# Performance work log

Hardware: AMD Instinct MI355X
Metric: run time of the kernel (lower is better)

## Reference

```python
import jax, jax.numpy as jnp
import numpy as np

IOU_THRESHOLD = 0.5  # default iou_threshold of nms/class_spec_nms


def _nms_keep_mask(boxes, scores, iou_threshold):
    """Faithful port of the hand-rolled greedy NMS.

    The torch version builds a variable-length index list; here we return the
    equivalent fixed-shape boolean keep mask over the N boxes (jit-friendly).
    """
    n = scores.shape[0]
    x1, y1, x2, y2 = boxes[:, 0], boxes[:, 1], boxes[:, 2], boxes[:, 3]
    areas = (x2 - x1) * (y2 - y1)                       # [N]
    # pairwise intersection via broadcasted min/max (same math as the matmul-
    # with-ones trick in the source, without materializing the ones matrices)
    xi = jnp.minimum(x2[:, None], x2[None, :]) - jnp.maximum(x1[:, None], x1[None, :])
    yi = jnp.minimum(y2[:, None], y2[None, :]) - jnp.maximum(y1[:, None], y1[None, :])
    inter = jnp.maximum(xi, 0.0) * jnp.maximum(yi, 0.0)  # [N,N]
    iou = inter / (areas[:, None] + areas[None, :] - inter)

    first_max = scores.max()
    first_min = scores.min()
    curr_idx0 = jnp.argmax(scores)

    # carry: (candidate mask, working scores copy, keep mask, curr max, curr idx)
    init = (scores < first_max, scores, jnp.zeros((n,), dtype=bool), first_max, curr_idx0)

    def cond(state):
        mask, _, _, cmax, _ = state
        return jnp.any(mask) & (cmax >= first_min)

    def body(state):
        mask, sc, keep, cmax, cidx = state
        mask = mask & (iou[cidx] <= iou_threshold)   # suppress overlaps with current max
        mask = mask.at[cidx].set(False)
        keep = keep.at[cidx].set(True)               # keep current max
        sc = jnp.where(mask, sc, first_min - 1.0)    # kill suppressed scores
        cidx = jnp.argmax(sc)
        return mask, sc, keep, sc[cidx], cidx

    _, _, keep, _, _ = jax.lax.while_loop(cond, body, init)
    return keep


def setup_inputs() -> dict:
    key = jax.random.key(0)
    k1, k2, k3, k4, k5, k6 = jax.random.split(key, 6)
    N = 4096    # pre-NMS candidate boxes
    L = 16384   # p3 locations for a 1024x1024 image at stride 8 (128*128)
    xy = jax.random.uniform(k1, (N, 2), dtype=jnp.float32) * 900.0
    wh = jax.random.uniform(k2, (N, 2), dtype=jnp.float32) * 100.0 + 1.0
    boxes = jnp.concatenate([xy, xy + wh], axis=1)          # valid x1<x2, y1<y2
    scores = jax.random.uniform(k3, (N,), dtype=jnp.float32)
    class_ids = jax.random.randint(k4, (N,), 0, 80, dtype=jnp.int32)
    locations = jax.random.uniform(k5, (L, 2), dtype=jnp.float32) * 1024.0
    deltas = jax.random.uniform(k6, (L, 4), dtype=jnp.float32)  # positive gt deltas
    return {"boxes": boxes, "scores": scores, "class_ids": class_ids,
            "locations": locations, "deltas": deltas, "stride": 8}


def reference(boxes, scores, class_ids, locations, deltas, stride):
    # ---- class_spec_nms: class-offset trick then plain NMS ----
    max_coordinate = boxes.max()
    offsets = class_ids.astype(boxes.dtype) * (max_coordinate + 1.0)
    boxes_for_nms = boxes + offsets[:, None]
    keep_mask = _nms_keep_mask(boxes_for_nms, scores, IOU_THRESHOLD)

    # ---- fcos_apply_deltas_to_locations ----
    clipped = jnp.maximum(deltas, 0.0)
    s = jnp.asarray(stride, dtype=deltas.dtype)
    px, py = locations[:, 0], locations[:, 1]
    pred_boxes = jnp.stack([px - clipped[:, 0] * s,
                            py - clipped[:, 1] * s,
                            px + clipped[:, 2] * s,
                            py + clipped[:, 3] * s], axis=1)  # [L,4]

    # ---- fcos_make_centerness_targets ----
    lr_min = jnp.minimum(deltas[:, 0], deltas[:, 2])
    tb_min = jnp.minimum(deltas[:, 1], deltas[:, 3])
    lr_max = jnp.maximum(deltas[:, 0], deltas[:, 2])
    tb_max = jnp.maximum(deltas[:, 1], deltas[:, 3])
    centerness = jnp.sqrt((lr_min * tb_min) / (lr_max * tb_max))
    centerness = jnp.where(jnp.all(deltas == -1.0, axis=1), -1.0, centerness)

    pred_out = jnp.concatenate([pred_boxes, centerness[:, None]], axis=1)  # [L,5]
    return keep_mask, pred_out
```

## Files before the change

### kernel.cpp

```cpp
#include <hip/hip_runtime.h>
#include <stdint.h>

#define NB 4096
#define NBLK 64
#define LLOC 16384
#define IOU_THR 0.5f
#define ECAP 1024
#define RANKB 256
#define NTRI (NBLK * (NBLK + 1) / 2)

typedef unsigned long long u64;

__device__ __forceinline__ u64 readlane64(u64 v, int lane) {
    unsigned lo = (unsigned)__builtin_amdgcn_readlane((int)(unsigned)(v & 0xffffffffull), lane);
    unsigned hi = (unsigned)__builtin_amdgcn_readlane((int)(unsigned)(v >> 32), lane);
    return ((u64)hi << 32) | (u64)lo;
}

__global__ void __launch_bounds__(256) fused_front(
        const float* __restrict__ boxes, const float* __restrict__ scores,
        const float* __restrict__ loc, const float* __restrict__ deltas,
        const int* __restrict__ stride_p,
        float* __restrict__ pred_out, float* __restrict__ maxc,
        int* __restrict__ sidx, int* __restrict__ counts) {
    __shared__ __align__(16) float sh[NB];
    __shared__ float red[4];
    int blk = blockIdx.x;
    int t = threadIdx.x;

    if (blk < 64) {
        int i = blk * 256 + t;
        float s = (float)stride_p[0];
        float2 p = ((const float2*)loc)[i];
        float4 d = ((const float4*)deltas)[i];
        float c0 = fmaxf(d.x, 0.f), c1 = fmaxf(d.y, 0.f);
        float c2 = fmaxf(d.z, 0.f), c3 = fmaxf(d.w, 0.f);
        float b0 = p.x - c0 * s;
        float b1 = p.y - c1 * s;
        float b2 = p.x + c2 * s;
        float b3 = p.y + c3 * s;
        float lr_min = fminf(d.x, d.z), tb_min = fminf(d.y, d.w);
        float lr_max = fmaxf(d.x, d.z), tb_max = fmaxf(d.y, d.w);
        float cent = sqrtf((lr_min * tb_min) / (lr_max * tb_max));
        if (d.x == -1.f && d.y == -1.f && d.z == -1.f && d.w == -1.f) cent = -1.f;
        float* o = pred_out + (size_t)i * 5;
        o[0] = b0; o[1] = b1; o[2] = b2; o[3] = b3; o[4] = cent;
    } else if (blk < 64 + RANKB) {
        for (int i = t; i < NB; i += 256) sh[i] = scores[i];
        __syncthreads();
        int wave = t >> 6, lane = t & 63;
        int base = (blk - 64) * 16 + wave * 4;
        float my0 = sh[base + 0], my1 = sh[base + 1];
        float my2 = sh[base + 2], my3 = sh[base + 3];
        int c0 = 0, c1 = 0, c2 = 0, c3 = 0;
#pragma unroll 8
        for (int k = 0; k < 64; ++k) {
            int j = lane + k * 64;
            float sj = sh[j];
            c0 += (sj > my0) || (sj == my0 && j < base + 0);
            c1 += (sj > my1) || (sj == my1 && j < base + 1);
            c2 += (sj > my2) || (sj == my2 && j < base + 2);
            c3 += (sj > my3) || (sj == my3 && j < base + 3);
        }
        for (int o = 32; o > 0; o >>= 1) {
            c0 += __shfl_down(c0, o); c1 += __shfl_down(c1, o);
            c2 += __shfl_down(c2, o); c3 += __shfl_down(c3, o);
        }
        if (lane == 0) {
            sidx[c0] = base + 0; sidx[c1] = base + 1;
            sidx[c2] = base + 2; sidx[c3] = base + 3;
        }
    } else {
        if (t < NBLK) counts[t] = 0;
        float m = -3.0e38f;
        for (int i = t; i < NB * 4; i += 256) m = fmaxf(m, boxes[i]);
        for (int o = 32; o > 0; o >>= 1) m = fmaxf(m, __shfl_down(m, o));
        if ((t & 63) == 0) red[t >> 6] = m;
        __syncthreads();
        if (t == 0) *maxc = fmaxf(fmaxf(red[0], red[1]), fmaxf(red[2], red[3]));
    }
}

__global__ void __launch_bounds__(64) edge_kernel(
        const float* __restrict__ boxes, const int* __restrict__ cls,
        const float* __restrict__ maxc, const int* __restrict__ sidx,
        int* __restrict__ counts, uint4* __restrict__ entries,
        u64* __restrict__ dcol) {
    int idx = blockIdx.x, r = 0;
    while (idx >= NBLK - r) { idx -= NBLK - r; ++r; }
    int c = r + idx;

    __shared__ float4 cb[64];
    __shared__ float ca[64];
    int t = threadIdx.x;
    float mc1 = maxc[0] + 1.0f;

    int jr = sidx[r * 64 + t];
    float offr = (float)cls[jr] * mc1;
    float4 rb = ((const float4*)boxes)[jr];
    rb.x += offr; rb.y += offr; rb.z += offr; rb.w += offr;
    float ra = (rb.z - rb.x) * (rb.w - rb.y);

    if (c == r) {
        cb[t] = rb; ca[t] = ra;
    } else {
        int jc = sidx[c * 64 + t];
        float offc = (float)cls[jc] * mc1;
        float4 b = ((const float4*)boxes)[jc];
        b.x += offc; b.y += offc; b.z += offc; b.w += offc;
        cb[t] = b; ca[t] = (b.z - b.x) * (b.w - b.y);
    }
    __syncthreads();

    u64 w = 0;
#pragma unroll 8
    for (int j = 0; j < 64; ++j) {
        float4 b = cb[j];
        float xi = fminf(rb.z, b.z) - fmaxf(rb.x, b.x);
        float yi = fminf(rb.w, b.w) - fmaxf(rb.y, b.y);
        float inter = fmaxf(xi, 0.f) * fmaxf(yi, 0.f);
        float iou = inter / (ra + ca[j] - inter);
        w |= (u64)(iou > IOU_THR) << j;
    }
    if (c == r) {
        w &= ~(1ull << t);
        dcol[r * 64 + t] = w;
    } else if (w) {
        int slot = atomicAdd(&counts[r], 1);
        if (slot < ECAP)
            entries[r * ECAP + slot] =
                make_uint4((unsigned)(t | (c << 8)), 0u,
                           (unsigned)(w & 0xffffffffull), (unsigned)(w >> 32));
    }
}

__global__ void __launch_bounds__(256) scan_kernel(
        const int* __restrict__ counts, const uint4* __restrict__ entries,
        const u64* __restrict__ dcol, const int* __restrict__ sidx,
        float* __restrict__ keep_out) {
    __shared__ u64 rem_lds[NBLK];
    __shared__ u64 kept_lds[NBLK];
    const int t = threadIdx.x;
    const int lane = t & 63;

    if (t < 64) {
        rem_lds[t] = 0;
        int cnt_l = counts[lane];
        u64 keptall_w = 0;
        u64 self = 1ull << lane;

        uint4 cur = entries[lane];
        uint4 n1  = entries[ECAP + lane];
        u64 cw_cur = dcol[lane];
        u64 cw_n1  = dcol[64 + lane];
        for (int b = 0; b < NBLK; ++b) {
            uint4 n2; u64 cw_n2;
            if (b < NBLK - 2) {
                n2    = entries[(u64)(b + 2) * ECAP + lane];
                cw_n2 = dcol[(b + 2) * 64 + lane];
            }

            int cnt = __builtin_amdgcn_readlane(cnt_l, b);
            if (cnt > ECAP) cnt = ECAP;

            u64 colw = self | cw_cur;

            u64 rem = rem_lds[b];
            u64 avail = ~rem;
            u64 edges = colw & avail & ~self;
            u64 involved = __ballot(edges != 0ull) & avail;
            u64 keptm = avail & ~involved;
            u64 sub = involved;
            while (sub) {
                int i = (int)__builtin_ctzll(sub);
                keptm |= 1ull << i;
                u64 ci = readlane64(colw, i);
                sub &= ~(ci | (1ull << i));
            }
            if (lane == b) keptall_w = keptm;

            if (lane < cnt) {
                int l = cur.x & 255, c = cur.x >> 8;
                if ((keptm >> l) & 1ull)
                    atomicOr(&rem_lds[c], ((u64)cur.w << 32) | cur.z);
            }
            for (int e = 64; e < cnt; e += 64) {
                int ee = e + lane;
                if (ee < cnt) {
                    uint4 x = entries[(u64)b * ECAP + ee];
                    int l = x.x & 255, c = x.x >> 8;
                    if ((keptm >> l) & 1ull)
                        atomicOr(&rem_lds[c], ((u64)x.w << 32) | x.z);
                }
            }
            cur = n1; n1 = n2; cw_cur = cw_n1; cw_n1 = cw_n2;
        }
        kept_lds[lane] = keptall_w;
    }
    __syncthreads();

    int w = t >> 6;
#pragma unroll
    for (int k = 0; k < 16; ++k) {
        int bb = w + k * 4;
        u64 kw = kept_lds[bb];
        int idx = sidx[bb * 64 + lane];
        keep_out[idx] = ((kw >> lane) & 1ull) ? 1.0f : 0.0f;
    }
}

extern "C" void kernel_launch(void* const* d_in, const int* in_sizes, int n_in,
                              void* d_out, int out_size, void* d_ws, size_t ws_size,
                              hipStream_t stream) {
    const float* boxes   = (const float*)d_in[0];
    const float* scores  = (const float*)d_in[1];
    const int*   cls     = (const int*)d_in[2];
    const float* loc     = (const float*)d_in[3];
    const float* deltas  = (const float*)d_in[4];
    const int*   stride  = (const int*)d_in[5];

    float* out = (float*)d_out;
    float* keep_out = out;
    float* pred_out = out + NB;

    char* ws = (char*)d_ws;
    float* maxc    = (float*)ws;                     ws += 16;
    int*   sidx    = (int*)ws;                       ws += NB * sizeof(int);
    int*   counts  = (int*)ws;                       ws += NBLK * sizeof(int) + 16;
    uint4* entries = (uint4*)ws;                     ws += (size_t)NBLK * ECAP * sizeof(uint4);
    u64*   dcol    = (u64*)ws;

    fused_front<<<64 + RANKB + 1, 256, 0, stream>>>(boxes, scores, loc, deltas, stride,
                                                    pred_out, maxc, sidx, counts);
    edge_kernel<<<NTRI, 64, 0, stream>>>(boxes, cls, maxc, sidx, counts, entries, dcol);
    scan_kernel<<<1, 256, 0, stream>>>(counts, entries, dcol, sidx, keep_out);
}
```

Before: 108.4 us.

## Fuse three kernels into one cooperative kernel with grid-wide syncs

Replaces the three separate launches (front, edge, scan) with a single cooperative kernel of 256 blocks that uses grid.sync() between phases. Edge tiles are spread across waves with a grid-stride loop rather than one block per tile. The goal is to remove launch gaps and inter-kernel drain between the stages. In exchange it adds grid barrier cost and leaves the final scan to one block while the rest of the grid sits idle. It keeps a fallback to the old launches if the cooperative launch fails.

```diff
diff --git a/kernel.cpp b/kernel.cpp
--- a/kernel.cpp
+++ b/kernel.cpp
@@ -1,4 +1,5 @@
 #include <hip/hip_runtime.h>
+#include <hip/hip_cooperative_groups.h>
 #include <stdint.h>
 
 #define NB 4096
@@ -8,13 +9,205 @@
 #define ECAP 1024
 #define RANKB 256
 #define NTRI (NBLK * (NBLK + 1) / 2)
-
+#define GRID 256
+
+namespace cg = cooperative_groups;
 typedef unsigned long long u64;
 
 __device__ __forceinline__ u64 readlane64(u64 v, int lane) {
     unsigned lo = (unsigned)__builtin_amdgcn_readlane((int)(unsigned)(v & 0xffffffffull), lane);
     unsigned hi = (unsigned)__builtin_amdgcn_readlane((int)(unsigned)(v >> 32), lane);
     return ((u64)hi << 32) | (u64)lo;
+}
+
+__global__ void __launch_bounds__(256) fcos_fused(
+        const float* __restrict__ boxes, const float* __restrict__ scores,
+        const int* __restrict__ cls, const float* __restrict__ loc,
+        const float* __restrict__ deltas, const int* __restrict__ stride_p,
+        float* __restrict__ keep_out, float* __restrict__ pred_out,
+        float* __restrict__ maxc, int* __restrict__ sidx,
+        int* __restrict__ counts, uint4* __restrict__ entries,
+        u64* __restrict__ dcol) {
+    __shared__ __align__(16) float sh[NB];
+    __shared__ float4 cbs[4][64];
+    __shared__ float cas[4][64];
+    __shared__ u64 rem_lds[NBLK];
+    __shared__ u64 kept_lds[NBLK];
+    __shared__ float red[4];
+
+    cg::grid_group gridg = cg::this_grid();
+    const int blk = blockIdx.x;
+    const int t = threadIdx.x;
+    const int wave = t >> 6, lane = t & 63;
+
+    if (blk < 64) {
+        int i = blk * 256 + t;
+        float s = (float)stride_p[0];
+        float2 p = ((const float2*)loc)[i];
+        float4 d = ((const float4*)deltas)[i];
+        float c0 = fmaxf(d.x, 0.f), c1 = fmaxf(d.y, 0.f);
+        float c2 = fmaxf(d.z, 0.f), c3 = fmaxf(d.w, 0.f);
+        float b0 = p.x - c0 * s;
+        float b1 = p.y - c1 * s;
+        float b2 = p.x + c2 * s;
+        float b3 = p.y + c3 * s;
+        float lr_min = fminf(d.x, d.z), tb_min = fminf(d.y, d.w);
+        float lr_max = fmaxf(d.x, d.z), tb_max = fmaxf(d.y, d.w);
+        float cent = sqrtf((lr_min * tb_min) / (lr_max * tb_max));
+        if (d.x == -1.f && d.y == -1.f && d.z == -1.f && d.w == -1.f) cent = -1.f;
+        float* o = pred_out + (size_t)i * 5;
+        o[0] = b0; o[1] = b1; o[2] = b2; o[3] = b3; o[4] = cent;
+    }
+    if (blk == 64) {
+        if (t < NBLK) counts[t] = 0;
+        float m = -3.0e38f;
+        for (int i = t; i < NB * 4; i += 256) m = fmaxf(m, boxes[i]);
+        for (int o = 32; o > 0; o >>= 1) m = fmaxf(m, __shfl_down(m, o));
+        if ((t & 63) == 0) red[t >> 6] = m;
+        __syncthreads();
+        if (t == 0) *maxc = fmaxf(fmaxf(red[0], red[1]), fmaxf(red[2], red[3]));
+    }
+    {
+        for (int i = t; i < NB; i += 256) sh[i] = scores[i];
+        __syncthreads();
+        int base = blk * 16 + wave * 4;
+        float my0 = sh[base + 0], my1 = sh[base + 1];
+        float my2 = sh[base + 2], my3 = sh[base + 3];
+        int c0 = 0, c1 = 0, c2 = 0, c3 = 0;
+#pragma unroll 8
+        for (int k = 0; k < 64; ++k) {
+            int j = lane + k * 64;
+            float sj = sh[j];
+            c0 += (sj > my0) || (sj == my0 && j < base + 0);
+            c1 += (sj > my1) || (sj == my1 && j < base + 1);
+            c2 += (sj > my2) || (sj == my2 && j < base + 2);
+            c3 += (sj > my3) || (sj == my3 && j < base + 3);
+        }
+        for (int o = 32; o > 0; o >>= 1) {
+            c0 += __shfl_down(c0, o); c1 += __shfl_down(c1, o);
+            c2 += __shfl_down(c2, o); c3 += __shfl_down(c3, o);
+        }
+        if (lane == 0) {
+            sidx[c0] = base + 0; sidx[c1] = base + 1;
+            sidx[c2] = base + 2; sidx[c3] = base + 3;
+        }
+    }
+
+    gridg.sync();
+
+    {
+        float mc1 = maxc[0] + 1.0f;
+        float4* cb = cbs[wave];
+        float* ca = cas[wave];
+        int wgid = blk * 4 + wave;
+        for (int tile = wgid; tile < NTRI; tile += GRID * 4) {
+            int idx = tile, r = 0;
+            while (idx >= NBLK - r) { idx -= NBLK - r; ++r; }
+            int c = r + idx;
+
+            int jr = sidx[r * 64 + lane];
+            float offr = (float)cls[jr] * mc1;
+            float4 rb = ((const float4*)boxes)[jr];
+            rb.x += offr; rb.y += offr; rb.z += offr; rb.w += offr;
+            float ra = (rb.z - rb.x) * (rb.w - rb.y);
+
+            if (c == r) {
+                cb[lane] = rb; ca[lane] = ra;
+            } else {
+                int jc = sidx[c * 64 + lane];
+                float offc = (float)cls[jc] * mc1;
+                float4 b = ((const float4*)boxes)[jc];
+                b.x += offc; b.y += offc; b.z += offc; b.w += offc;
+                cb[lane] = b; ca[lane] = (b.z - b.x) * (b.w - b.y);
+            }
+
+            u64 w = 0;
+#pragma unroll 8
+            for (int j = 0; j < 64; ++j) {
+                float4 b = cb[j];
+                float xi = fminf(rb.z, b.z) - fmaxf(rb.x, b.x);
+                float yi = fminf(rb.w, b.w) - fmaxf(rb.y, b.y);
+                float inter = fmaxf(xi, 0.f) * fmaxf(yi, 0.f);
+                float iou = inter / (ra + ca[j] - inter);
+                w |= (u64)(iou > IOU_THR) << j;
+            }
+            if (c == r) {
+                w &= ~(1ull << lane);
+                dcol[r * 64 + lane] = w;
+            } else if (w) {
+                int slot = atomicAdd(&counts[r], 1);
+                if (slot < ECAP)
+                    entries[r * ECAP + slot] =
+                        make_uint4((unsigned)(lane | (c << 8)), 0u,
+                                   (unsigned)(w & 0xffffffffull), (unsigned)(w >> 32));
+            }
+        }
+    }
+
+    gridg.sync();
+
+    if (blk == 0) {
+        if (t < 64) {
+            rem_lds[t] = 0;
+            int cnt_l = counts[t];
+            u64 keptall_w = 0;
+            u64 self = 1ull << t;
+            uint4 cur = entries[t];
+            uint4 n1  = entries[ECAP + t];
+            u64 cw_cur = dcol[t];
+            u64 cw_n1  = dcol[64 + t];
+            for (int b = 0; b < NBLK; ++b) {
+                uint4 n2; u64 cw_n2;
+                if (b < NBLK - 2) {
+                    n2    = entries[(u64)(b + 2) * ECAP + t];
+                    cw_n2 = dcol[(b + 2) * 64 + t];
+                }
+                int cnt = __builtin_amdgcn_readlane(cnt_l, b);
+                if (cnt > ECAP) cnt = ECAP;
+
+                u64 colw = self | cw_cur;
+
+                u64 rem = rem_lds[b];
+                u64 avail = ~rem;
+                u64 edges = colw & avail & ~self;
+                u64 involved = __ballot(edges != 0ull) & avail;
+                u64 keptm = avail & ~involved;
+                u64 sub = involved;
+                while (sub) {
+                    int i = (int)__builtin_ctzll(sub);
+                    keptm |= 1ull << i;
+                    u64 ci = readlane64(colw, i);
+                    sub &= ~(ci | (1ull << i));
+                }
+                if (t == b) keptall_w = keptm;
+
+                if (t < cnt) {
+                    int l = cur.x & 255, c = cur.x >> 8;
+                    if ((keptm >> l) & 1ull)
+                        atomicOr(&rem_lds[c], ((u64)cur.w << 32) | cur.z);
+                }
+                for (int e = 64; e < cnt; e += 64) {
+                    int ee = e + t;
+                    if (ee < cnt) {
+                        uint4 x = entries[(u64)b * ECAP + ee];
+                        int l = x.x & 255, c = x.x >> 8;
+                        if ((keptm >> l) & 1ull)
+                            atomicOr(&rem_lds[c], ((u64)x.w << 32) | x.z);
+                    }
+                }
+                cur = n1; n1 = n2; cw_cur = cw_n1; cw_n1 = cw_n2;
+            }
+            kept_lds[t] = keptall_w;
+        }
+        __syncthreads();
+#pragma unroll
+        for (int k = 0; k < 16; ++k) {
+            int bb = wave + k * 4;
+            u64 kw = kept_lds[bb];
+            int idx = sidx[bb * 64 + lane];
+            keep_out[idx] = ((kw >> lane) & 1ull) ? 1.0f : 0.0f;
+        }
+    }
 }
 
 __global__ void __launch_bounds__(256) fused_front(
@@ -148,7 +341,6 @@
         int cnt_l = counts[lane];
         u64 keptall_w = 0;
         u64 self = 1ull << lane;
-
         uint4 cur = entries[lane];
         uint4 n1  = entries[ECAP + lane];
         u64 cw_cur = dcol[lane];
@@ -159,12 +351,9 @@
                 n2    = entries[(u64)(b + 2) * ECAP + lane];
                 cw_n2 = dcol[(b + 2) * 64 + lane];
             }
-
             int cnt = __builtin_amdgcn_readlane(cnt_l, b);
             if (cnt > ECAP) cnt = ECAP;
-
             u64 colw = self | cw_cur;
-
             u64 rem = rem_lds[b];
             u64 avail = ~rem;
             u64 edges = colw & avail & ~self;
@@ -178,7 +367,6 @@
                 sub &= ~(ci | (1ull << i));
             }
             if (lane == b) keptall_w = keptm;
-
             if (lane < cnt) {
                 int l = cur.x & 255, c = cur.x >> 8;
                 if ((keptm >> l) & 1ull)
@@ -230,8 +418,17 @@
     uint4* entries = (uint4*)ws;                     ws += (size_t)NBLK * ECAP * sizeof(uint4);
     u64*   dcol    = (u64*)ws;
 
-    fused_front<<<64 + RANKB + 1, 256, 0, stream>>>(boxes, scores, loc, deltas, stride,
-                                                    pred_out, maxc, sidx, counts);
-    edge_kernel<<<NTRI, 64, 0, stream>>>(boxes, cls, maxc, sidx, counts, entries, dcol);
-    scan_kernel<<<1, 256, 0, stream>>>(counts, entries, dcol, sidx, keep_out);
-}
+    void* args[] = {(void*)&boxes, (void*)&scores, (void*)&cls, (void*)&loc,
+                    (void*)&deltas, (void*)&stride, (void*)&keep_out,
+                    (void*)&pred_out, (void*)&maxc, (void*)&sidx,
+                    (void*)&counts, (void*)&entries, (void*)&dcol};
+    hipError_t err = hipLaunchCooperativeKernel((const void*)fcos_fused,
+                                                dim3(GRID), dim3(256),
+                                                args, 0, stream);
+    if (err != hipSuccess) {
+        fused_front<<<64 + RANKB + 1, 256, 0, stream>>>(boxes, scores, loc, deltas,
+                                                        stride, pred_out, maxc, sidx, counts);
+        edge_kernel<<<NTRI, 64, 0, stream>>>(boxes, cls, maxc, sidx, counts, entries, dcol);
+        scan_kernel<<<1, 256, 0, stream>>>(counts, entries, dcol, sidx, keep_out);
+    }
+}
```

Result: slower. 183.2 us (+69.0%).

## Fuse edge and scan kernels via last-block-done pattern, move pred to edge launch

Applied to the files above, without the earlier changes.

Merges the edge-building kernel and the single-block scan kernel into one launch: each 256-thread block now handles four triangle tiles (one per wave), and the last block to finish, detected through an atomic counter stored after the per-row counts, runs the greedy scan. The FCOS box and centerness computation moves from the front kernel into extra blocks of this fused launch. This removes one kernel launch and its dependency gap. The cost is a grid-wide atomic with threadfences, and the serial scan now runs inside whichever block happens to finish last.

```diff
diff --git a/kernel.cpp b/kernel.cpp
--- a/kernel.cpp
+++ b/kernel.cpp
@@ -8,6 +8,8 @@
 #define ECAP 1024
 #define RANKB 256
 #define NTRI (NBLK * (NBLK + 1) / 2)
+#define EBLK 520
+#define PREDB 64
 
 typedef unsigned long long u64;
 
@@ -17,19 +19,65 @@
     return ((u64)hi << 32) | (u64)lo;
 }
 
-__global__ void __launch_bounds__(256) fused_front(
+__global__ void __launch_bounds__(256) front_kernel(
         const float* __restrict__ boxes, const float* __restrict__ scores,
-        const float* __restrict__ loc, const float* __restrict__ deltas,
-        const int* __restrict__ stride_p,
-        float* __restrict__ pred_out, float* __restrict__ maxc,
-        int* __restrict__ sidx, int* __restrict__ counts) {
+        float* __restrict__ maxc, int* __restrict__ sidx,
+        int* __restrict__ counts ) {
     __shared__ __align__(16) float sh[NB];
     __shared__ float red[4];
     int blk = blockIdx.x;
     int t = threadIdx.x;
 
-    if (blk < 64) {
-        int i = blk * 256 + t;
+    if (blk < RANKB) {
+        for (int i = t; i < NB; i += 256) sh[i] = scores[i];
+        __syncthreads();
+        int wave = t >> 6, lane = t & 63;
+        int base = blk * 16 + wave * 4;
+        float my0 = sh[base + 0], my1 = sh[base + 1];
+        float my2 = sh[base + 2], my3 = sh[base + 3];
+        int c0 = 0, c1 = 0, c2 = 0, c3 = 0;
+#pragma unroll 8
+        for (int k = 0; k < 64; ++k) {
+            int j = lane + k * 64;
+            float sj = sh[j];
+            c0 += (sj > my0) || (sj == my0 && j < base + 0);
+            c1 += (sj > my1) || (sj == my1 && j < base + 1);
+            c2 += (sj > my2) || (sj == my2 && j < base + 2);
+            c3 += (sj > my3) || (sj == my3 && j < base + 3);
+        }
+        for (int o = 32; o > 0; o >>= 1) {
+            c0 += __shfl_down(c0, o); c1 += __shfl_down(c1, o);
+            c2 += __shfl_down(c2, o); c3 += __shfl_down(c3, o);
+        }
+        if (lane == 0) {
+            sidx[c0] = base + 0; sidx[c1] = base + 1;
+            sidx[c2] = base + 2; sidx[c3] = base + 3;
+        }
+    } else {
+        if (t < NBLK + 1) counts[t] = 0;
+        float m = -3.0e38f;
+        for (int i = t; i < NB * 4; i += 256) m = fmaxf(m, boxes[i]);
+        for (int o = 32; o > 0; o >>= 1) m = fmaxf(m, __shfl_down(m, o));
+        if ((t & 63) == 0) red[t >> 6] = m;
+        __syncthreads();
+        if (t == 0) *maxc = fmaxf(fmaxf(red[0], red[1]), fmaxf(red[2], red[3]));
+    }
+}
+
+__global__ void __launch_bounds__(256) edgescan_kernel(
+        const float* __restrict__ boxes, const int* __restrict__ cls,
+        const float* __restrict__ maxc, const int* __restrict__ sidx,
+        int* __restrict__ counts, uint4* __restrict__ entries,
+        u64* __restrict__ dcol,
+        const float* __restrict__ loc, const float* __restrict__ deltas,
+        const int* __restrict__ stride_p, float* __restrict__ pred_out,
+        float* __restrict__ keep_out) {
+    const int blk = blockIdx.x;
+    const int t = threadIdx.x;
+    const int wave = t >> 6, lane = t & 63;
+
+    if (blk >= EBLK) {
+        int i = (blk - EBLK) * 256 + t;
         float s = (float)stride_p[0];
         float2 p = ((const float2*)loc)[i];
         float4 d = ((const float4*)deltas)[i];
@@ -45,121 +93,87 @@
         if (d.x == -1.f && d.y == -1.f && d.z == -1.f && d.w == -1.f) cent = -1.f;
         float* o = pred_out + (size_t)i * 5;
         o[0] = b0; o[1] = b1; o[2] = b2; o[3] = b3; o[4] = cent;
-    } else if (blk < 64 + RANKB) {
-        for (int i = t; i < NB; i += 256) sh[i] = scores[i];
-        __syncthreads();
-        int wave = t >> 6, lane = t & 63;
-        int base = (blk - 64) * 16 + wave * 4;
-        float my0 = sh[base + 0], my1 = sh[base + 1];
-        float my2 = sh[base + 2], my3 = sh[base + 3];
-        int c0 = 0, c1 = 0, c2 = 0, c3 = 0;
-#pragma unroll 8
-        for (int k = 0; k < 64; ++k) {
-            int j = lane + k * 64;
-            float sj = sh[j];
-            c0 += (sj > my0) || (sj == my0 && j < base + 0);
-            c1 += (sj > my1) || (sj == my1 && j < base + 1);
-            c2 += (sj > my2) || (sj == my2 && j < base + 2);
-            c3 += (sj > my3) || (sj == my3 && j < base + 3);
-        }
-        for (int o = 32; o > 0; o >>= 1) {
-            c0 += __shfl_down(c0, o); c1 += __shfl_down(c1, o);
-            c2 += __shfl_down(c2, o); c3 += __shfl_down(c3, o);
-        }
-        if (lane == 0) {
-            sidx[c0] = base + 0; sidx[c1] = base + 1;
-            sidx[c2] = base + 2; sidx[c3] = base + 3;
-        }
-    } else {
-        if (t < NBLK) counts[t] = 0;
-        float m = -3.0e38f;
-        for (int i = t; i < NB * 4; i += 256) m = fmaxf(m, boxes[i]);
-        for (int o = 32; o > 0; o >>= 1) m = fmaxf(m, __shfl_down(m, o));
-        if ((t & 63) == 0) red[t >> 6] = m;
-        __syncthreads();
-        if (t == 0) *maxc = fmaxf(fmaxf(red[0], red[1]), fmaxf(red[2], red[3]));
-    }
-}
-
-__global__ void __launch_bounds__(64) edge_kernel(
-        const float* __restrict__ boxes, const int* __restrict__ cls,
-        const float* __restrict__ maxc, const int* __restrict__ sidx,
-        int* __restrict__ counts, uint4* __restrict__ entries,
-        u64* __restrict__ dcol) {
-    int idx = blockIdx.x, r = 0;
-    while (idx >= NBLK - r) { idx -= NBLK - r; ++r; }
-    int c = r + idx;
-
-    __shared__ float4 cb[64];
-    __shared__ float ca[64];
-    int t = threadIdx.x;
-    float mc1 = maxc[0] + 1.0f;
-
-    int jr = sidx[r * 64 + t];
-    float offr = (float)cls[jr] * mc1;
-    float4 rb = ((const float4*)boxes)[jr];
-    rb.x += offr; rb.y += offr; rb.z += offr; rb.w += offr;
-    float ra = (rb.z - rb.x) * (rb.w - rb.y);
-
-    if (c == r) {
-        cb[t] = rb; ca[t] = ra;
-    } else {
-        int jc = sidx[c * 64 + t];
-        float offc = (float)cls[jc] * mc1;
-        float4 b = ((const float4*)boxes)[jc];
-        b.x += offc; b.y += offc; b.z += offc; b.w += offc;
-        cb[t] = b; ca[t] = (b.z - b.x) * (b.w - b.y);
-    }
-    __syncthreads();
-
-    u64 w = 0;
-#pragma unroll 8
-    for (int j = 0; j < 64; ++j) {
-        float4 b = cb[j];
-        float xi = fminf(rb.z, b.z) - fmaxf(rb.x, b.x);
-        float yi = fminf(rb.w, b.w) - fmaxf(rb.y, b.y);
-        float inter = fmaxf(xi, 0.f) * fmaxf(yi, 0.f);
-        float iou = inter / (ra + ca[j] - inter);
-        w |= (u64)(iou > IOU_THR) << j;
-    }
-    if (c == r) {
-        w &= ~(1ull << t);
-        dcol[r * 64 + t] = w;
-    } else if (w) {
-        int slot = atomicAdd(&counts[r], 1);
-        if (slot < ECAP)
-            entries[r * ECAP + slot] =
-                make_uint4((unsigned)(t | (c << 8)), 0u,
-                           (unsigned)(w & 0xffffffffull), (unsigned)(w >> 32));
-    }
-}
-
-__global__ void __launch_bounds__(256) scan_kernel(
-        const int* __restrict__ counts, const uint4* __restrict__ entries,
-        const u64* __restrict__ dcol, const int* __restrict__ sidx,
-        float* __restrict__ keep_out) {
+        return;
+    }
+
+    __shared__ float4 cbs[4][64];
+    __shared__ float cas[4][64];
     __shared__ u64 rem_lds[NBLK];
     __shared__ u64 kept_lds[NBLK];
-    const int t = threadIdx.x;
-    const int lane = t & 63;
+    __shared__ int last_flag;
+    int* done = counts + NBLK;
+
+    {
+        int idx = blk * 4 + wave, r = 0;
+        while (idx >= NBLK - r) { idx -= NBLK - r; ++r; }
+        int c = r + idx;
+        float mc1 = maxc[0] + 1.0f;
+        float4* cb = cbs[wave];
+        float* ca = cas[wave];
+
+        int jr = sidx[r * 64 + lane];
+        float offr = (float)cls[jr] * mc1;
+        float4 rb = ((const float4*)boxes)[jr];
+        rb.x += offr; rb.y += offr; rb.z += offr; rb.w += offr;
+        float ra = (rb.z - rb.x) * (rb.w - rb.y);
+
+        if (c == r) {
+            cb[lane] = rb; ca[lane] = ra;
+        } else {
+            int jc = sidx[c * 64 + lane];
+            float offc = (float)cls[jc] * mc1;
+            float4 b = ((const float4*)boxes)[jc];
+            b.x += offc; b.y += offc; b.z += offc; b.w += offc;
+            cb[lane] = b; ca[lane] = (b.z - b.x) * (b.w - b.y);
+        }
+
+        u64 w = 0;
+#pragma unroll 8
+        for (int j = 0; j < 64; ++j) {
+            float4 b = cb[j];
+            float xi = fminf(rb.z, b.z) - fmaxf(rb.x, b.x);
+            float yi = fminf(rb.w, b.w) - fmaxf(rb.y, b.y);
+            float inter = fmaxf(xi, 0.f) * fmaxf(yi, 0.f);
+            float iou = inter / (ra + ca[j] - inter);
+            w |= (u64)(iou > IOU_THR) << j;
+        }
+        if (c == r) {
+            w &= ~(1ull << lane);
+            dcol[r * 64 + lane] = w;
+        } else if (w) {
+            int slot = atomicAdd(&counts[r], 1);
+            if (slot < ECAP)
+                entries[r * ECAP + slot] =
+                    make_uint4((unsigned)(lane | (c << 8)), 0u,
+                               (unsigned)(w & 0xffffffffull), (unsigned)(w >> 32));
+        }
+    }
+
+    __syncthreads();
+    if (t == 0) {
+        __threadfence();
+        int tk = atomicAdd(done, 1);
+        last_flag = (tk == EBLK - 1);
+    }
+    __syncthreads();
+    if (!last_flag) return;
+    __threadfence();
 
     if (t < 64) {
         rem_lds[t] = 0;
-        int cnt_l = counts[lane];
+        int cnt_l = counts[t];
         u64 keptall_w = 0;
-        u64 self = 1ull << lane;
-
-        uint4 cur = entries[lane];
-        uint4 n1  = entries[ECAP + lane];
-        u64 cw_cur = dcol[lane];
-        u64 cw_n1  = dcol[64 + lane];
+        u64 self = 1ull << t;
+        uint4 cur = entries[t];
+        uint4 n1  = entries[ECAP + t];
+        u64 cw_cur = dcol[t];
+        u64 cw_n1  = dcol[64 + t];
         for (int b = 0; b < NBLK; ++b) {
             uint4 n2; u64 cw_n2;
             if (b < NBLK - 2) {
-                n2    = entries[(u64)(b + 2) * ECAP + lane];
-                cw_n2 = dcol[(b + 2) * 64 + lane];
-            }
-
+                n2    = entries[(u64)(b + 2) * ECAP + t];
+                cw_n2 = dcol[(b + 2) * 64 + t];
+            }
             int cnt = __builtin_amdgcn_readlane(cnt_l, b);
             if (cnt > ECAP) cnt = ECAP;
 
@@ -177,15 +191,15 @@
                 u64 ci = readlane64(colw, i);
                 sub &= ~(ci | (1ull << i));
             }
-            if (lane == b) keptall_w = keptm;
-
-            if (lane < cnt) {
+            if (t == b) keptall_w = keptm;
+
+            if (t < cnt) {
                 int l = cur.x & 255, c = cur.x >> 8;
                 if ((keptm >> l) & 1ull)
                     atomicOr(&rem_lds[c], ((u64)cur.w << 32) | cur.z);
             }
             for (int e = 64; e < cnt; e += 64) {
-                int ee = e + lane;
+                int ee = e + t;
                 if (ee < cnt) {
                     uint4 x = entries[(u64)b * ECAP + ee];
                     int l = x.x & 255, c = x.x >> 8;
@@ -195,14 +209,13 @@
             }
             cur = n1; n1 = n2; cw_cur = cw_n1; cw_n1 = cw_n2;
         }
-        kept_lds[lane] = keptall_w;
+        kept_lds[t] = keptall_w;
     }
     __syncthreads();
 
-    int w = t >> 6;
 #pragma unroll
     for (int k = 0; k < 16; ++k) {
-        int bb = w + k * 4;
+        int bb = wave + k * 4;
         u64 kw = kept_lds[bb];
         int idx = sidx[bb * 64 + lane];
         keep_out[idx] = ((kw >> lane) & 1ull) ? 1.0f : 0.0f;
@@ -230,8 +243,9 @@
     uint4* entries = (uint4*)ws;                     ws += (size_t)NBLK * ECAP * sizeof(uint4);
     u64*   dcol    = (u64*)ws;
 
-    fused_front<<<64 + RANKB + 1, 256, 0, stream>>>(boxes, scores, loc, deltas, stride,
-                                                    pred_out, maxc, sidx, counts);
-    edge_kernel<<<NTRI, 64, 0, stream>>>(boxes, cls, maxc, sidx, counts, entries, dcol);
-    scan_kernel<<<1, 256, 0, stream>>>(counts, entries, dcol, sidx, keep_out);
-}
+    front_kernel<<<RANKB + 1, 256, 0, stream>>>(boxes, scores, maxc, sidx, counts);
+    edgescan_kernel<<<EBLK + PREDB, 256, 0, stream>>>(boxes, cls, maxc, sidx,
+                                                      counts, entries, dcol,
+                                                      loc, deltas, stride,
+                                                      pred_out, keep_out);
+}
```

After: 116.1 us. +7.1%, slower.
